# Performance work log

Measured on AMD Instinct MI355X. Metric: run time of the kernel, lower is better.

## Reference

```python
import jax, jax.numpy as jnp
import numpy as np

D_MODEL = 2048
N_HEADS = 16
N_KV_HEADS = 2
HEAD_DIM = D_MODEL // N_HEADS  # 128
N_REP = N_HEADS // N_KV_HEADS  # 8
SCALE = HEAD_DIM ** -0.5


def setup_inputs() -> dict:
    key = jax.random.key(0)
    ks = jax.random.split(key, 5)
    B, N = 2, 2048
    x = jax.random.normal(ks[0], (B, N, D_MODEL), dtype=jnp.float32)
    # weights stored as [in, out] (math identical to torch Linear x @ W.T)
    s = D_MODEL ** -0.5
    Wq = jax.random.normal(ks[1], (D_MODEL, D_MODEL), dtype=jnp.float32) * s
    Wk = jax.random.normal(ks[2], (D_MODEL, N_KV_HEADS * HEAD_DIM), dtype=jnp.float32) * s
    Wv = jax.random.normal(ks[3], (D_MODEL, N_KV_HEADS * HEAD_DIM), dtype=jnp.float32) * s
    Wo = jax.random.normal(ks[4], (D_MODEL, D_MODEL), dtype=jnp.float32) * s
    return {"x": x, "Wq": Wq, "Wk": Wk, "Wv": Wv, "Wo": Wo}


def reference(x, Wq, Wk, Wv, Wo):
    B, N, C = x.shape
    q = (x @ Wq).reshape(B, N, N_HEADS, HEAD_DIM).transpose(0, 2, 1, 3)      # [B,H,N,hd]
    k = (x @ Wk).reshape(B, N, N_KV_HEADS, HEAD_DIM).transpose(0, 2, 1, 3)   # [B,Hkv,N,hd]
    v = (x @ Wv).reshape(B, N, N_KV_HEADS, HEAD_DIM).transpose(0, 2, 1, 3)
    if N_REP > 1:
        k = jnp.repeat(k, N_REP, axis=1)  # [B,H,N,hd]
        v = jnp.repeat(v, N_REP, axis=1)
    attn = jnp.einsum('bhnd,bhmd->bhnm', q, k) * SCALE
    attn = jax.nn.softmax(attn, axis=-1)
    out = jnp.einsum('bhnm,bhmd->bhnd', attn, v)
    out = out.transpose(0, 2, 1, 3).reshape(B, N, C)
    return out @ Wo
```

## Files before the change

### kernel.cpp

```cpp
#include <hip/hip_runtime.h>

typedef unsigned short u16;
typedef __attribute__((ext_vector_type(4))) float floatx4;
typedef __attribute__((ext_vector_type(8))) __bf16 bf16x8;
typedef __attribute__((ext_vector_type(8))) u16 u16x8;

#define D_MODEL 2048
#define SEQ     2048
#define NH      16
#define NKV     2
#define HD      128
#define QKVN    2560
#define SCALE   0.08838834764831845f
#define QSCALE  (0.08838834764831845f * 1.4426950408889634f)
#define THR_LOG2 11.5f

__device__ __forceinline__ u16 f2bf(float f) {
    unsigned int x = __float_as_uint(f);
    return (u16)((x + 0x7fffu + ((x >> 16) & 1u)) >> 16);
}
__device__ __forceinline__ u16 cvt_scale(float f, float s) { return f2bf(f * s); }
__device__ __forceinline__ u16 cvt_scale(u16 f, float)     { return f; }

__device__ __forceinline__ void gload16(const u16* g, u16* l) {
    __builtin_amdgcn_global_load_lds((const __attribute__((address_space(1))) void*)g,
                                     (__attribute__((address_space(3))) void*)l, 16, 0, 0);
}

__global__ void f2b_k(const float* __restrict__ src, u16* __restrict__ dst, long n)
{
    long i = ((long)blockIdx.x * blockDim.x + threadIdx.x) * 8;
    if (i >= n) return;
    float4 a = *(const float4*)(src + i);
    float4 b = *(const float4*)(src + i + 4);
    u16x8 o;
    o[0] = f2bf(a.x); o[1] = f2bf(a.y); o[2] = f2bf(a.z); o[3] = f2bf(a.w);
    o[4] = f2bf(b.x); o[5] = f2bf(b.y); o[6] = f2bf(b.z); o[7] = f2bf(b.w);
    *(u16x8*)(dst + i) = o;
}

template <typename T>
__global__ void tr_k(const T* __restrict__ src, u16* __restrict__ dst,
                     int ld_s, int ld_d, long sbs, long dbs, float scale)
{
    __shared__ T tile[32][33];
    src += (long)blockIdx.z * sbs;
    dst += (long)blockIdx.z * dbs;
    int c0 = blockIdx.x * 32, r0 = blockIdx.y * 32;
    int tx = threadIdx.x, ty = threadIdx.y;
#pragma unroll
    for (int i = 0; i < 32; i += 8)
        tile[ty + i][tx] = src[(long)(r0 + ty + i) * ld_s + c0 + tx];
    __syncthreads();
#pragma unroll
    for (int i = 0; i < 32; i += 8)
        dst[(long)(c0 + ty + i) * ld_d + r0 + tx] = cvt_scale(tile[tx][ty + i], scale);
}

template <bool F32OUT>
__global__ __launch_bounds__(256, 2) void gemm_bt_k(
    const u16* __restrict__ A, const u16* __restrict__ Bt, void* __restrict__ Cv,
    int K, int lda, int ldb, int ldc)
{
    __shared__ __align__(16) u16 As[128 * 64];
    __shared__ __align__(16) u16 Bs[128 * 64];
    const int tid  = threadIdx.x;
    const int wave = tid >> 6, lane = tid & 63;
    const int quad = lane >> 4, l16 = lane & 15;
    const long bm = (long)blockIdx.x * 128;
    const long bn = (long)blockIdx.y * 128;
    const int wr = (wave >> 1) * 64;
    const int wc = (wave & 1) * 64;

    floatx4 acc[4][4] = {};

    for (long k0 = 0; k0 < K; k0 += 64) {
#pragma unroll
        for (int t = 0; t < 4; ++t) {
            int c = tid + t * 256;
            int row = c >> 3, sl = c & 7;
            int kc = sl ^ (row & 7);
            gload16(A + (bm + row) * lda + k0 + kc * 8,
                    As + ((tid & ~63) + t * 256) * 8);
        }
#pragma unroll
        for (int t = 0; t < 4; ++t) {
            int c = tid + t * 256;
            int row = c >> 3, sl = c & 7;
            int kc = sl ^ (row & 7);
            gload16(Bt + (bn + row) * ldb + k0 + kc * 8,
                    Bs + ((tid & ~63) + t * 256) * 8);
        }
        __syncthreads();

#pragma unroll
        for (int ks = 0; ks < 2; ++ks) {
            bf16x8 af[4], bfr[4];
#pragma unroll
            for (int mt = 0; mt < 4; ++mt) {
                int r  = wr + mt * 16 + l16;
                int ch = (ks * 4 + quad) ^ (r & 7);
                af[mt] = *(const bf16x8*)(As + r * 64 + ch * 8);
            }
#pragma unroll
            for (int nt = 0; nt < 4; ++nt) {
                int r  = wc + nt * 16 + l16;
                int ch = (ks * 4 + quad) ^ (r & 7);
                bfr[nt] = *(const bf16x8*)(Bs + r * 64 + ch * 8);
            }
#pragma unroll
            for (int mt = 0; mt < 4; ++mt)
#pragma unroll
                for (int nt = 0; nt < 4; ++nt)
                    acc[mt][nt] = __builtin_amdgcn_mfma_f32_16x16x32_bf16(
                        af[mt], bfr[nt], acc[mt][nt], 0, 0, 0);
        }
        __syncthreads();
    }

#pragma unroll
    for (int mt = 0; mt < 4; ++mt)
#pragma unroll
        for (int nt = 0; nt < 4; ++nt)
#pragma unroll
            for (int r = 0; r < 4; ++r) {
                long row = bm + wr + mt * 16 + quad * 4 + r;
                long col = bn + wc + nt * 16 + l16;
                if (F32OUT) ((float*)Cv)[row * ldc + col] = acc[mt][nt][r];
                else        ((u16*)Cv)[row * ldc + col]   = f2bf(acc[mt][nt][r]);
            }
}

#define KTILE (64 * 128)
#define VTILE (128 * 64)

__global__ __launch_bounds__(256, 2) void attn_k(
    const u16* __restrict__ QKV, const u16* __restrict__ Vt, u16* __restrict__ Out)
{
    __shared__ __align__(16) u16 smem[2 * KTILE + 2 * VTILE + 128 * 64];

    const int tid  = threadIdx.x;
    const int wave = tid >> 6, lane = tid & 63;
    const int quad = lane >> 4, l16 = lane & 15;
    const int qt = blockIdx.x, h = blockIdx.y, b = blockIdx.z;
    const int kvh = h >> 3;

    const long qrow0 = (long)b * SEQ + (long)qt * 128;
    const u16* Qbase = QKV + qrow0 * QKVN + h * HD;
    const u16* Kbase = QKV + (long)b * SEQ * QKVN + D_MODEL + kvh * HD;
    const u16* Vbase = Vt + ((long)b * NKV + kvh) * (long)HD * SEQ;
    u16* const P = smem + 2 * KTILE + 2 * VTILE;

#pragma unroll
    for (int t = 0; t < 8; ++t) {
        int c = tid + t * 256;
        int row = c >> 4, sl = c & 15;
        int dc = sl ^ (row & 15);
        gload16(Qbase + (long)row * QKVN + dc * 8, smem + ((tid & ~63) + t * 256) * 8);
    }
    __syncthreads();

    bf16x8 qa[2][4];
#pragma unroll
    for (int mt = 0; mt < 2; ++mt)
#pragma unroll
        for (int ks = 0; ks < 4; ++ks) {
            int r  = wave * 32 + mt * 16 + l16;
            int ch = (ks * 4 + quad) ^ (r & 15);
            qa[mt][ks] = *(const bf16x8*)(smem + r * 128 + ch * 8);
        }
    __syncthreads();

    floatx4 o[2][8] = {};
    float m_run[2] = { -1e30f, -1e30f };
    float l_run[2] = { 0.f, 0.f };

    {
        u16* Kn = smem;
        u16* Vn = smem + 2 * KTILE;
#pragma unroll
        for (int t = 0; t < 4; ++t) {
            int c = tid + t * 256;
            int row = c >> 4, sl = c & 15;
            int dc = sl ^ (row & 15);
            gload16(Kbase + (long)row * QKVN + dc * 8, Kn + ((tid & ~63) + t * 256) * 8);
        }
#pragma unroll
        for (int t = 0; t < 4; ++t) {
            int c = tid + t * 256;
            int row = c >> 3, sl = c & 7;
            int kc = sl ^ (row & 7);
            gload16(Vbase + (long)row * SEQ + kc * 8, Vn + ((tid & ~63) + t * 256) * 8);
        }
    }
    __syncthreads();

    for (int t = 0; t < SEQ / 64; ++t) {
        const int cur = t & 1;
        const u16* Kc = smem + cur * KTILE;
        const u16* Vc = smem + 2 * KTILE + cur * VTILE;

        if (t + 1 < SEQ / 64) {
            u16* Kn = smem + (cur ^ 1) * KTILE;
            u16* Vn = smem + 2 * KTILE + (cur ^ 1) * VTILE;
            const long k0n = (long)(t + 1) * 64;
#pragma unroll
            for (int tt = 0; tt < 4; ++tt) {
                int c = tid + tt * 256;
                int row = c >> 4, sl = c & 15;
                int dc = sl ^ (row & 15);
                gload16(Kbase + (k0n + row) * QKVN + dc * 8,
                        Kn + ((tid & ~63) + tt * 256) * 8);
            }
#pragma unroll
            for (int tt = 0; tt < 4; ++tt) {
                int c = tid + tt * 256;
                int row = c >> 3, sl = c & 7;
                int kc = sl ^ (row & 7);
                gload16(Vbase + (long)row * SEQ + k0n + kc * 8,
                        Vn + ((tid & ~63) + tt * 256) * 8);
            }
        }

        floatx4 s[2][4] = {};
        __builtin_amdgcn_s_setprio(1);
#pragma unroll
        for (int ks = 0; ks < 4; ++ks) {
            bf16x8 kb[4];
#pragma unroll
            for (int nt = 0; nt < 4; ++nt) {
                int r  = nt * 16 + l16;
                int ch = (ks * 4 + quad) ^ (r & 15);
                kb[nt] = *(const bf16x8*)(Kc + r * 128 + ch * 8);
            }
#pragma unroll
            for (int mt = 0; mt < 2; ++mt)
#pragma unroll
                for (int nt = 0; nt < 4; ++nt)
                    s[mt][nt] = __builtin_amdgcn_mfma_f32_16x16x32_bf16(
                        kb[nt], qa[mt][ks], s[mt][nt], 0, 0, 0);
        }
        __builtin_amdgcn_s_setprio(0);

        float alf[2];
        int need = 0;
#pragma unroll
        for (int mt = 0; mt < 2; ++mt) {
            float ma = fmaxf(fmaxf(s[mt][0][0], s[mt][0][1]), fmaxf(s[mt][0][2], s[mt][0][3]));
            float mb = fmaxf(fmaxf(s[mt][1][0], s[mt][1][1]), fmaxf(s[mt][1][2], s[mt][1][3]));
            float mc = fmaxf(fmaxf(s[mt][2][0], s[mt][2][1]), fmaxf(s[mt][2][2], s[mt][2][3]));
            float md = fmaxf(fmaxf(s[mt][3][0], s[mt][3][1]), fmaxf(s[mt][3][2], s[mt][3][3]));
            float mx = fmaxf(fmaxf(ma, mb), fmaxf(mc, md));
            mx = fmaxf(mx, __shfl_xor(mx, 16));
            mx = fmaxf(mx, __shfl_xor(mx, 32));
            float mold = m_run[mt];
            float mnew = (mx > mold + THR_LOG2) ? mx : mold;
            float al = __builtin_amdgcn_exp2f(mold - mnew);
            m_run[mt] = mnew;
#pragma unroll
            for (int nt = 0; nt < 4; ++nt)
#pragma unroll
                for (int r = 0; r < 4; ++r)
                    s[mt][nt][r] = __builtin_amdgcn_exp2f(s[mt][nt][r] - mnew);
            float ta = (s[mt][0][0] + s[mt][0][1]) + (s[mt][0][2] + s[mt][0][3]);
            float tb = (s[mt][1][0] + s[mt][1][1]) + (s[mt][1][2] + s[mt][1][3]);
            float tc = (s[mt][2][0] + s[mt][2][1]) + (s[mt][2][2] + s[mt][2][3]);
            float td = (s[mt][3][0] + s[mt][3][1]) + (s[mt][3][2] + s[mt][3][3]);
            float sum = (ta + tb) + (tc + td);
            sum += __shfl_xor(sum, 16);
            sum += __shfl_xor(sum, 32);
            l_run[mt] = l_run[mt] * al + sum;
            alf[mt] = al;
            need |= (al != 1.f);
        }
        if (__any(need)) {
#pragma unroll
            for (int mt = 0; mt < 2; ++mt)
#pragma unroll
                for (int r = 0; r < 4; ++r) {
                    float alr = __shfl(alf[mt], (lane & 48) | (quad * 4 + r));
#pragma unroll
                    for (int dt = 0; dt < 8; ++dt) o[mt][dt][r] *= alr;
                }
        }

#pragma unroll
        for (int mt = 0; mt < 2; ++mt) {
            int row = wave * 32 + mt * 16 + l16;
            int swz = (row >> 1) & 7;
            u16* base = P + row * 64 + (quad & 1) * 4;
#pragma unroll
            for (int nt = 0; nt < 4; ++nt) {
                unsigned int lo, hi;
                asm("v_cvt_pk_bf16_f32 %0, %1, %2"
                    : "=v"(lo) : "v"(s[mt][nt][0]), "v"(s[mt][nt][1]));
                asm("v_cvt_pk_bf16_f32 %0, %1, %2"
                    : "=v"(hi) : "v"(s[mt][nt][2]), "v"(s[mt][nt][3]));
                int chunk = (nt * 2 + (quad >> 1)) ^ swz;
                uint2 val; val.x = lo; val.y = hi;
                *(uint2*)(base + chunk * 8) = val;
            }
        }

        __builtin_amdgcn_s_setprio(1);
#pragma unroll
        for (int ks = 0; ks < 2; ++ks) {
            bf16x8 pa[2];
#pragma unroll
            for (int mt = 0; mt < 2; ++mt) {
                int row = wave * 32 + mt * 16 + l16;
                int chk = (ks * 4 + quad) ^ ((row >> 1) & 7);
                pa[mt] = *(const bf16x8*)(P + row * 64 + chk * 8);
            }
#pragma unroll
            for (int dt = 0; dt < 8; ++dt) {
                int r  = dt * 16 + l16;
                int ch = (ks * 4 + quad) ^ (r & 7);
                bf16x8 vb = *(const bf16x8*)(Vc + r * 64 + ch * 8);
#pragma unroll
                for (int mt = 0; mt < 2; ++mt)
                    o[mt][dt] = __builtin_amdgcn_mfma_f32_16x16x32_bf16(
                        pa[mt], vb, o[mt][dt], 0, 0, 0);
            }
        }
        __builtin_amdgcn_s_setprio(0);
        __syncthreads();
    }

#pragma unroll
    for (int mt = 0; mt < 2; ++mt)
#pragma unroll
        for (int r = 0; r < 4; ++r) {
            float linv = __shfl(l_run[mt], (lane & 48) | (quad * 4 + r));
            float inv = 1.f / linv;
            long row = qrow0 + wave * 32 + mt * 16 + quad * 4 + r;
#pragma unroll
            for (int dt = 0; dt < 8; ++dt)
                Out[row * D_MODEL + h * HD + dt * 16 + l16] = f2bf(o[mt][dt][r] * inv);
        }
}

extern "C" void kernel_launch(void* const* d_in, const int* in_sizes, int n_in,
                              void* d_out, int out_size, void* d_ws, size_t ws_size,
                              hipStream_t stream)
{
    const float* X  = (const float*)d_in[0];
    const float* Wq = (const float*)d_in[1];
    const float* Wk = (const float*)d_in[2];
    const float* Wv = (const float*)d_in[3];
    const float* Wo = (const float*)d_in[4];
    float* out = (float*)d_out;

    u16* Xb    = (u16*)d_ws;
    u16* attn  = Xb;
    u16* WtQKV = Xb + (long)4096 * D_MODEL;
    u16* WtO   = WtQKV + (long)QKVN * D_MODEL;
    u16* QKV   = WtO + (long)D_MODEL * D_MODEL;
    u16* Vt    = QKV + (long)4096 * QKVN;

    f2b_k<<<dim3(4096), 256, 0, stream>>>(X, Xb, (long)4096 * D_MODEL);

    dim3 tb(32, 8);
    tr_k<float><<<dim3(64, 64, 1), tb, 0, stream>>>(Wq, WtQKV, 2048, 2048, 0, 0, QSCALE);
    tr_k<float><<<dim3(8, 64, 1), tb, 0, stream>>>(Wk, WtQKV + 2048L * 2048, 256, 2048, 0, 0, 1.f);
    tr_k<float><<<dim3(8, 64, 1), tb, 0, stream>>>(Wv, WtQKV + 2304L * 2048, 256, 2048, 0, 0, 1.f);
    tr_k<float><<<dim3(64, 64, 1), tb, 0, stream>>>(Wo, WtO, 2048, 2048, 0, 0, 1.f);

    gemm_bt_k<false><<<dim3(32, 20), 256, 0, stream>>>(Xb, WtQKV, QKV, 2048, 2048, 2048, QKVN);

    tr_k<u16><<<dim3(8, 64, 2), tb, 0, stream>>>(QKV + 2304, Vt, QKVN, 2048,
                                                 (long)SEQ * QKVN, 256L * 2048, 1.f);

    attn_k<<<dim3(16, NH, 2), 256, 0, stream>>>(QKV, Vt, attn);

    gemm_bt_k<true><<<dim3(32, 16), 256, 0, stream>>>(attn, WtO, out, 2048, 2048, 2048, 2048);
}
```

Before: 290.7 us.

## Interleave per-tile softmax with PV MFMAs and start from a static running max

The running max now starts at a fixed log2-domain value instead of -inf. Rescaling of the scores, the row sum and the output accumulator only happens when a row's max exceeds it by the threshold, and that check is made per m-tile under a wave-wide vote. The softmax, the P store and the PV MFMAs are restructured to run per m-tile, so the exp/convert work of one tile can overlap the matrix work of the other. V fragments loaded for the first tile are kept in registers and reused for the second tile. The P LDS swizzle also changes. The aim is to cut redundant exp and rescale work and idle gaps between the VALU and MFMA phases, at the cost of about 64 extra VGPRs for the held V fragments, which risks lower occupancy or spills.

```diff
diff --git a/kernel.cpp b/kernel.cpp
--- a/kernel.cpp
+++ b/kernel.cpp
@@ -14,6 +14,7 @@
 #define SCALE   0.08838834764831845f
 #define QSCALE  (0.08838834764831845f * 1.4426950408889634f)
 #define THR_LOG2 11.5f
+#define M_STATIC 20.0f
 
 __device__ __forceinline__ u16 f2bf(float f) {
     unsigned int x = __float_as_uint(f);
@@ -172,7 +173,7 @@
     __syncthreads();
 
     floatx4 o[2][8] = {};
-    float m_run[2] = { -1e30f, -1e30f };
+    float m_run[2] = { M_STATIC, M_STATIC };
     float l_run[2] = { 0.f, 0.f };
 
     {
@@ -242,10 +243,11 @@
         }
         __builtin_amdgcn_s_setprio(0);
 
-        float alf[2];
-        int need = 0;
+        bf16x8 vb[2][8];
+
 #pragma unroll
         for (int mt = 0; mt < 2; ++mt) {
+            float mold = m_run[mt];
             float ma = fmaxf(fmaxf(s[mt][0][0], s[mt][0][1]), fmaxf(s[mt][0][2], s[mt][0][3]));
             float mb = fmaxf(fmaxf(s[mt][1][0], s[mt][1][1]), fmaxf(s[mt][1][2], s[mt][1][3]));
             float mc = fmaxf(fmaxf(s[mt][2][0], s[mt][2][1]), fmaxf(s[mt][2][2], s[mt][2][3]));
@@ -253,15 +255,11 @@
             float mx = fmaxf(fmaxf(ma, mb), fmaxf(mc, md));
             mx = fmaxf(mx, __shfl_xor(mx, 16));
             mx = fmaxf(mx, __shfl_xor(mx, 32));
-            float mold = m_run[mt];
-            float mnew = (mx > mold + THR_LOG2) ? mx : mold;
-            float al = __builtin_amdgcn_exp2f(mold - mnew);
-            m_run[mt] = mnew;
 #pragma unroll
             for (int nt = 0; nt < 4; ++nt)
 #pragma unroll
                 for (int r = 0; r < 4; ++r)
-                    s[mt][nt][r] = __builtin_amdgcn_exp2f(s[mt][nt][r] - mnew);
+                    s[mt][nt][r] = __builtin_amdgcn_exp2f(s[mt][nt][r] - mold);
             float ta = (s[mt][0][0] + s[mt][0][1]) + (s[mt][0][2] + s[mt][0][3]);
             float tb = (s[mt][1][0] + s[mt][1][1]) + (s[mt][1][2] + s[mt][1][3]);
             float tc = (s[mt][2][0] + s[mt][2][1]) + (s[mt][2][2] + s[mt][2][3]);
@@ -269,61 +267,66 @@
             float sum = (ta + tb) + (tc + td);
             sum += __shfl_xor(sum, 16);
             sum += __shfl_xor(sum, 32);
-            l_run[mt] = l_run[mt] * al + sum;
-            alf[mt] = al;
-            need |= (al != 1.f);
-        }
-        if (__any(need)) {
-#pragma unroll
-            for (int mt = 0; mt < 2; ++mt)
+            if (__any(mx > mold + THR_LOG2)) {
+                float mnew = (mx > mold + THR_LOG2) ? mx : mold;
+                float f = __builtin_amdgcn_exp2f(mold - mnew);
+#pragma unroll
+                for (int nt = 0; nt < 4; ++nt)
+#pragma unroll
+                    for (int r = 0; r < 4; ++r) s[mt][nt][r] *= f;
+                sum *= f;
+                l_run[mt] *= f;
+                m_run[mt] = mnew;
 #pragma unroll
                 for (int r = 0; r < 4; ++r) {
-                    float alr = __shfl(alf[mt], (lane & 48) | (quad * 4 + r));
-#pragma unroll
-                    for (int dt = 0; dt < 8; ++dt) o[mt][dt][r] *= alr;
+                    float fr = __shfl(f, (lane & 48) | (quad * 4 + r));
+#pragma unroll
+                    for (int dt = 0; dt < 8; ++dt) o[mt][dt][r] *= fr;
                 }
-        }
-
-#pragma unroll
-        for (int mt = 0; mt < 2; ++mt) {
-            int row = wave * 32 + mt * 16 + l16;
-            int swz = (row >> 1) & 7;
-            u16* base = P + row * 64 + (quad & 1) * 4;
-#pragma unroll
-            for (int nt = 0; nt < 4; ++nt) {
-                unsigned int lo, hi;
-                asm("v_cvt_pk_bf16_f32 %0, %1, %2"
-                    : "=v"(lo) : "v"(s[mt][nt][0]), "v"(s[mt][nt][1]));
-                asm("v_cvt_pk_bf16_f32 %0, %1, %2"
-                    : "=v"(hi) : "v"(s[mt][nt][2]), "v"(s[mt][nt][3]));
-                int chunk = (nt * 2 + (quad >> 1)) ^ swz;
-                uint2 val; val.x = lo; val.y = hi;
-                *(uint2*)(base + chunk * 8) = val;
-            }
-        }
-
-        __builtin_amdgcn_s_setprio(1);
-#pragma unroll
-        for (int ks = 0; ks < 2; ++ks) {
-            bf16x8 pa[2];
-#pragma unroll
-            for (int mt = 0; mt < 2; ++mt) {
+            }
+            l_run[mt] += sum;
+
+            {
                 int row = wave * 32 + mt * 16 + l16;
-                int chk = (ks * 4 + quad) ^ ((row >> 1) & 7);
-                pa[mt] = *(const bf16x8*)(P + row * 64 + chk * 8);
-            }
-#pragma unroll
-            for (int dt = 0; dt < 8; ++dt) {
-                int r  = dt * 16 + l16;
-                int ch = (ks * 4 + quad) ^ (r & 7);
-                bf16x8 vb = *(const bf16x8*)(Vc + r * 64 + ch * 8);
-#pragma unroll
-                for (int mt = 0; mt < 2; ++mt)
-                    o[mt][dt] = __builtin_amdgcn_mfma_f32_16x16x32_bf16(
-                        pa[mt], vb, o[mt][dt], 0, 0, 0);
-            }
-        }
-        __builtin_amdgcn_s_setprio(0);
+                int swz = row & 7;
+                u16* base = P + row * 64 + (quad & 1) * 4;
+#pragma unroll
+                for (int nt = 0; nt < 4; ++nt) {
+                    unsigned int lo, hi;
+                    asm("v_cvt_pk_bf16_f32 %0, %1, %2"
+                        : "=v"(lo) : "v"(s[mt][nt][0]), "v"(s[mt][nt][1]));
+                    asm("v_cvt_pk_bf16_f32 %0, %1, %2"
+                        : "=v"(hi) : "v"(s[mt][nt][2]), "v"(s[mt][nt][3]));
+                    int chunk = (nt * 2 + (quad >> 1)) ^ swz;
+                    uint2 val; val.x = lo; val.y = hi;
+                    *(uint2*)(base + chunk * 8) = val;
+                }
+            }
+
+            __builtin_amdgcn_s_setprio(1);
+#pragma unroll
+            for (int ks = 0; ks < 2; ++ks) {
+                int row = wave * 32 + mt * 16 + l16;
+                int chk = (ks * 4 + quad) ^ (row & 7);
+                bf16x8 pa = *(const bf16x8*)(P + row * 64 + chk * 8);
+                if (mt == 0) {
+#pragma unroll
+                    for (int dt = 0; dt < 8; ++dt) {
+                        int r  = dt * 16 + l16;
+                        int ch = (ks * 4 + quad) ^ (r & 7);
+                        vb[ks][dt] = *(const bf16x8*)(Vc + r * 64 + ch * 8);
+                        o[0][dt] = __builtin_amdgcn_mfma_f32_16x16x32_bf16(
+                            pa, vb[ks][dt], o[0][dt], 0, 0, 0);
+                    }
+                } else {
+#pragma unroll
+                    for (int dt = 0; dt < 8; ++dt)
+                        o[1][dt] = __builtin_amdgcn_mfma_f32_16x16x32_bf16(
+                            pa, vb[ks][dt], o[1][dt], 0, 0, 0);
+                }
+            }
+            __builtin_amdgcn_s_setprio(0);
+        }
         __syncthreads();
     }
 
```

Result: slower. 298.9 us (+2.8%).
